# Optimization experiments

Measured on AMD Instinct MI355X. Metric: run time of the kernel, lower is better.

The kernel has to match this reference:

```python
import jax, jax.numpy as jnp
import numpy as np

# 4x4 Walsh-Hadamard matrix in natural (Hadamard/Kronecker) order: H4 = H2 (x) H2
_H4 = jnp.array([[1, 1, 1, 1],
                 [1, -1, 1, -1],
                 [1, 1, -1, -1],
                 [1, -1, -1, 1]], dtype=jnp.float32)

T = 16          # number of 2D WHT coefficients (4x4 block)
BLK = 4         # spatial block size


def _iwht_stream(trans, weight):
    """trans: (16, B, nH, nW, C); weight: (16, C, K) -> out: (B, 4*nH, 4*nW, K).

    Per-coefficient channel mixing in the transform domain, then inverse 2D
    Walsh-Hadamard transform (separable, scale 1/16) back to spatial domain.
    """
    _, B, nH, nW, C = trans.shape
    K = weight.shape[2]
    # transform-domain channel mixing: (t,b,h,w,c) x (t,c,k) -> (t,b,h,w,k)
    mixed = jnp.einsum('tbhwc,tck->tbhwk', trans, weight)
    # split coefficient index t = 4*u + v (row/col frequency)
    mixed = mixed.reshape(BLK, BLK, B, nH, nW, K)
    # inverse separable WHT: out[b,nh,i,nw,j,k] = (1/16) sum_{u,v} H4[i,u] H4[j,v] mixed[u,v,...]
    out = jnp.einsum('iu,jv,uvbhwk->bhiwjk', _H4, _H4, mixed) * (1.0 / 16.0)
    return out.reshape(B, nH * BLK, nW * BLK, K)


def setup_inputs() -> dict:
    key = jax.random.key(0)
    k1, k2, k3, k4 = jax.random.split(key, 4)
    B, nH, nW, C = 16, 28, 28, 64
    out_channels = 128
    K1 = out_channels // 2
    K2 = out_channels // 2 + out_channels % 2
    transIm1 = jax.random.normal(k1, (T, B, nH, nW, C), dtype=jnp.float32)
    transIm2 = jax.random.normal(k2, (T, B, nH, nW, C), dtype=jnp.float32)
    weight1 = jax.random.normal(k3, (T, C, K1), dtype=jnp.float32) * 0.02
    weight2 = jax.random.normal(k4, (T, C, K2), dtype=jnp.float32) * 0.02
    bias1 = jnp.zeros((1, 1, 1, K1), dtype=jnp.float32)
    bias2 = jnp.zeros((1, 1, 1, K2), dtype=jnp.float32)
    return {"transIm1": transIm1, "transIm2": transIm2,
            "weight1": weight1, "weight2": weight2,
            "bias1": bias1, "bias2": bias2}


def reference(transIm1, transIm2, weight1, weight2, bias1, bias2):
    out1 = _iwht_stream(transIm1, weight1) + bias1
    out2 = _iwht_stream(transIm2, weight2) + bias2
    return (out1, out2)
```

## Files before the change

kernel.cpp:

```cpp
#include <hip/hip_runtime.h>
#include <hip/hip_bf16.h>

typedef float f32x4 __attribute__((ext_vector_type(4)));
typedef short s16x8 __attribute__((ext_vector_type(8)));

#define NPIX       12544
#define OUT_STRIDE 12845056
#define NTILES     1568
#define GRIDX      512

__device__ __forceinline__ unsigned short f2bf(float x) {
    union { float f; unsigned u; } un; un.f = x;
    unsigned r = un.u + 0x7FFFu + ((un.u >> 16) & 1u);
    return (unsigned short)(r >> 16);
}

__device__ __forceinline__ short bfs(float x) {
    __hip_bfloat16 h = __float2bfloat16(x);
    return *reinterpret_cast<short*>(&h);
}

__device__ __forceinline__ void gload_lds16(const void* g, void* l) {
    __builtin_amdgcn_global_load_lds(
        (const __attribute__((address_space(1))) unsigned int*)g,
        (__attribute__((address_space(3))) unsigned int*)l, 16, 0, 0);
}

__global__ __launch_bounds__(256) void repack_weights(
        const float* __restrict__ w1, const float* __restrict__ w2,
        unsigned short* __restrict__ wf) {
    int gid = blockIdx.x * 256 + threadIdx.x;
    int k = gid & 63;
    int c = (gid >> 6) & 63;
    int t = (gid >> 12) & 15;
    int s = (gid >> 16) & 1;
    const float* __restrict__ w = s ? w2 : w1;
    float val = w[gid & 65535] * 0.0625f;
    int e = c & 7, lhi = (c >> 3) & 3, ks = c >> 5;
    int l  = lhi * 16 + (k & 15);
    int nt = k >> 4;
    int dst = ((((s * 16 + t) * 2 + ks) * 4 + nt) * 64 + l) * 8 + e;
    wf[dst] = f2bf(val);
}

__global__ __launch_bounds__(256, 2) void iwht_main(
        const float* __restrict__ trans1, const float* __restrict__ trans2,
        const unsigned short* __restrict__ wf,
        const float* __restrict__ bias1, const float* __restrict__ bias2,
        float* __restrict__ out) {
    __shared__ __align__(16) unsigned char lds[65536];

    const int tid  = threadIdx.x;
    const int wid  = tid >> 6;
    const int lane = tid & 63;
    const int lrow = lane & 15;
    const int lhi  = lane >> 4;
    const int bx   = blockIdx.x;

    const int   kk  = wid * 16 + lrow;
    const float bk1 = bias1[kk];
    const float bk2 = bias2[kk];

    const int M = ((NTILES - bx + GRIDX - 1) / GRIDX) * 2;

    const int qsrc = (wid >> 1) * 32 + lhi * 8 + (wid & 1) * 4;
    const s16x8* __restrict__ wbbase = (const s16x8*)wf + (size_t)wid * 64 + lane;

    auto stage_half = [&](int m) {
        const int tau = bx + (m >> 1) * GRIDX;
        const int hf  = m & 1;
        const int s   = (tau >= 784) ? 1 : 0;
        const int bid = tau - s * 784;
        const float* __restrict__ tr = s ? trans2 : trans1;
        const float* g0 = tr + (size_t)(bid * 16 + lrow) * 64 + qsrc;
        unsigned char* db = lds + (m & 1) * 32768 + wid * 1024;
        #pragma unroll
        for (int tt = 0; tt < 8; ++tt) {
            const int t = hf * 8 + tt;
            gload_lds16(g0 + (size_t)t * (NPIX * 64), db + tt * 4096);
        }
    };

    f32x4 o[4][4];
    #pragma unroll
    for (int i = 0; i < 4; ++i)
        #pragma unroll
        for (int j = 0; j < 4; ++j)
            o[i][j] = (f32x4){0.f, 0.f, 0.f, 0.f};

    s16x8 bH[16];

    stage_half(0);

    #pragma unroll 1
    for (int m = 0; m < M; ++m) {
        const int tau = bx + (m >> 1) * GRIDX;
        const int hf  = m & 1;
        const int s   = (tau >= 784) ? 1 : 0;
        const int bid = tau - s * 784;

        {
            const s16x8* __restrict__ wb = wbbase + (size_t)s * 8192;
            #pragma unroll
            for (int tt = 0; tt < 8; ++tt) {
                const int t = hf * 8 + tt;
                bH[tt * 2 + 0] = wb[(size_t)(t * 2 + 0) * 256];
                bH[tt * 2 + 1] = wb[(size_t)(t * 2 + 1) * 256];
            }
        }

        if (m + 1 < M) {
            stage_half(m + 1);
            asm volatile("s_waitcnt vmcnt(8)" ::: "memory");
        } else {
            asm volatile("s_waitcnt vmcnt(0)" ::: "memory");
        }
        __builtin_amdgcn_sched_barrier(0);
        __builtin_amdgcn_s_barrier();

        const unsigned char* __restrict__ hb = lds + (m & 1) * 32768;
        #pragma unroll
        for (int g = 0; g < 2; ++g) {
            f32x4 acc[4];
            #pragma unroll
            for (int v = 0; v < 4; ++v) {
                const int tt = g * 4 + v;
                const unsigned char* ab = hb + tt * 4096 + lane * 16;
                f32x4 q0 = *(const f32x4*)(ab);
                f32x4 q1 = *(const f32x4*)(ab + 1024);
                f32x4 q2 = *(const f32x4*)(ab + 2048);
                f32x4 q3 = *(const f32x4*)(ab + 3072);
                s16x8 a0, a1;
                #pragma unroll
                for (int e = 0; e < 4; ++e) {
                    a0[e] = bfs(q0[e]); a0[4 + e] = bfs(q1[e]);
                    a1[e] = bfs(q2[e]); a1[4 + e] = bfs(q3[e]);
                }
                f32x4 tacc = {0.f, 0.f, 0.f, 0.f};
                tacc = __builtin_amdgcn_mfma_f32_16x16x32_bf16(a0, bH[tt * 2 + 0], tacc, 0, 0, 0);
                tacc = __builtin_amdgcn_mfma_f32_16x16x32_bf16(a1, bH[tt * 2 + 1], tacc, 0, 0, 0);
                acc[v] = tacc;
            }
            f32x4 e0 = acc[0] + acc[1], e1 = acc[0] - acc[1];
            f32x4 e2 = acc[2] + acc[3], e3 = acc[2] - acc[3];
            f32x4 g0 = e0 + e2, g1 = e1 + e3, g2 = e0 - e2, g3 = e1 - e3;
            const int u = hf * 2 + g;
            const float s1 = (u & 1) ? -1.f : 1.f;
            const float s2 = (u & 2) ? -1.f : 1.f;
            const float s3 = s1 * s2;
            #pragma unroll
            for (int j = 0; j < 4; ++j) {
                f32x4 gj = (j == 0) ? g0 : ((j == 1) ? g1 : ((j == 2) ? g2 : g3));
                o[0][j] += gj;
                o[1][j] += s1 * gj;
                o[2][j] += s2 * gj;
                o[3][j] += s3 * gj;
            }
        }

        if (hf) {
            const float bk = s ? bk2 : bk1;
            const int bimg = bid / 49;
            const int hw0  = (bid % 49) * 16;
            float* __restrict__ outp = out + (s ? (size_t)OUT_STRIDE : 0);
            size_t rbase[4];
            #pragma unroll
            for (int r = 0; r < 4; ++r) {
                int hw = hw0 + lhi * 4 + r;
                int h = hw / 28, w = hw % 28;
                rbase[r] = ((size_t)(bimg * 112 + h * 4) * 112 + (w * 4)) * 64 + kk;
            }
            #pragma unroll
            for (int i = 0; i < 4; ++i)
                #pragma unroll
                for (int j = 0; j < 4; ++j) {
                    #pragma unroll
                    for (int r = 0; r < 4; ++r)
                        outp[rbase[r] + (size_t)((i * 112 + j) * 64)] = o[i][j][r] + bk;
                    o[i][j] = (f32x4){0.f, 0.f, 0.f, 0.f};
                }
        }

        __builtin_amdgcn_s_barrier();
    }
}

extern "C" void kernel_launch(void* const* d_in, const int* in_sizes, int n_in,
                              void* d_out, int out_size, void* d_ws, size_t ws_size,
                              hipStream_t stream) {
    const float* t1 = (const float*)d_in[0];
    const float* t2 = (const float*)d_in[1];
    const float* w1 = (const float*)d_in[2];
    const float* w2 = (const float*)d_in[3];
    const float* b1 = (const float*)d_in[4];
    const float* b2 = (const float*)d_in[5];
    unsigned short* wfrag = (unsigned short*)d_ws;
    float* out = (float*)d_out;

    repack_weights<<<dim3(512), dim3(256), 0, stream>>>(w1, w2, wfrag);
    iwht_main<<<dim3(GRIDX), dim3(256), 0, stream>>>(t1, t2, wfrag, b1, b2, out);
}
```

Before: 204.8 us.

## Use one tile per block and stage output through swizzled LDS for vector stores

Replaces the persistent 512-block loop with a 1568-block grid where each block handles a single tile, issuing both halves of its input loads up front. The output is first written into LDS with an XOR swizzle, then read back so each wave writes a full contiguous 1KB row with 16-byte stores, instead of the earlier scattered 4-byte stores. This targets poorly coalesced output writes and lets the hardware scheduler balance work across blocks. In exchange it adds an LDS round trip and extra barriers, and it loses cross-tile overlap of loads with compute inside a block.

After: 197.0 us. 3.8% less time.

```diff
diff --git a/kernel.cpp b/kernel.cpp
--- a/kernel.cpp
+++ b/kernel.cpp
@@ -6,8 +6,6 @@
 
 #define NPIX       12544
 #define OUT_STRIDE 12845056
-#define NTILES     1568
-#define GRIDX      512
 
 __device__ __forceinline__ unsigned short f2bf(float x) {
     union { float f; unsigned u; } un; un.f = x;
@@ -55,31 +53,44 @@
     const int lane = tid & 63;
     const int lrow = lane & 15;
     const int lhi  = lane >> 4;
-    const int bx   = blockIdx.x;
 
-    const int   kk  = wid * 16 + lrow;
-    const float bk1 = bias1[kk];
-    const float bk2 = bias2[kk];
-
-    const int M = ((NTILES - bx + GRIDX - 1) / GRIDX) * 2;
+    const int tau = blockIdx.x;
+    const int s   = (tau >= 784) ? 1 : 0;
+    const int bid = tau - s * 784;
+    const float* __restrict__ trans = s ? trans2 : trans1;
+    const int   kk = wid * 16 + lrow;
+    const float bk = (s ? bias2 : bias1)[kk];
 
     const int qsrc = (wid >> 1) * 32 + lhi * 8 + (wid & 1) * 4;
-    const s16x8* __restrict__ wbbase = (const s16x8*)wf + (size_t)wid * 64 + lane;
+    const float* __restrict__ g0 = trans + (size_t)(bid * 16 + lrow) * 64 + qsrc;
 
-    auto stage_half = [&](int m) {
-        const int tau = bx + (m >> 1) * GRIDX;
-        const int hf  = m & 1;
-        const int s   = (tau >= 784) ? 1 : 0;
-        const int bid = tau - s * 784;
-        const float* __restrict__ tr = s ? trans2 : trans1;
-        const float* g0 = tr + (size_t)(bid * 16 + lrow) * 64 + qsrc;
-        unsigned char* db = lds + (m & 1) * 32768 + wid * 1024;
-        #pragma unroll
-        for (int tt = 0; tt < 8; ++tt) {
-            const int t = hf * 8 + tt;
-            gload_lds16(g0 + (size_t)t * (NPIX * 64), db + tt * 4096);
-        }
-    };
+    #pragma unroll
+    for (int tt = 0; tt < 8; ++tt)
+        gload_lds16(g0 + (size_t)tt * (NPIX * 64), lds + wid * 1024 + tt * 4096);
+
+    const s16x8* __restrict__ wb = (const s16x8*)wf + (size_t)s * 8192 + wid * 64 + lane;
+    s16x8 bE[16];
+    #pragma unroll
+    for (int tt = 0; tt < 8; ++tt) {
+        bE[tt * 2 + 0] = wb[(size_t)(tt * 2 + 0) * 256];
+        bE[tt * 2 + 1] = wb[(size_t)(tt * 2 + 1) * 256];
+    }
+
+    #pragma unroll
+    for (int tt = 0; tt < 8; ++tt)
+        gload_lds16(g0 + (size_t)(8 + tt) * (NPIX * 64),
+                    lds + 32768 + wid * 1024 + tt * 4096);
+
+    asm volatile("s_waitcnt vmcnt(8)" ::: "memory");
+    __builtin_amdgcn_sched_barrier(0);
+    __builtin_amdgcn_s_barrier();
+
+    s16x8 bO[16];
+    #pragma unroll
+    for (int tt = 0; tt < 8; ++tt) {
+        bO[tt * 2 + 0] = wb[(size_t)((8 + tt) * 2 + 0) * 256];
+        bO[tt * 2 + 1] = wb[(size_t)((8 + tt) * 2 + 1) * 256];
+    }
 
     f32x4 o[4][4];
     #pragma unroll
@@ -88,37 +99,7 @@
         for (int j = 0; j < 4; ++j)
             o[i][j] = (f32x4){0.f, 0.f, 0.f, 0.f};
 
-    s16x8 bH[16];
-
-    stage_half(0);
-
-    #pragma unroll 1
-    for (int m = 0; m < M; ++m) {
-        const int tau = bx + (m >> 1) * GRIDX;
-        const int hf  = m & 1;
-        const int s   = (tau >= 784) ? 1 : 0;
-        const int bid = tau - s * 784;
-
-        {
-            const s16x8* __restrict__ wb = wbbase + (size_t)s * 8192;
-            #pragma unroll
-            for (int tt = 0; tt < 8; ++tt) {
-                const int t = hf * 8 + tt;
-                bH[tt * 2 + 0] = wb[(size_t)(t * 2 + 0) * 256];
-                bH[tt * 2 + 1] = wb[(size_t)(t * 2 + 1) * 256];
-            }
-        }
-
-        if (m + 1 < M) {
-            stage_half(m + 1);
-            asm volatile("s_waitcnt vmcnt(8)" ::: "memory");
-        } else {
-            asm volatile("s_waitcnt vmcnt(0)" ::: "memory");
-        }
-        __builtin_amdgcn_sched_barrier(0);
-        __builtin_amdgcn_s_barrier();
-
-        const unsigned char* __restrict__ hb = lds + (m & 1) * 32768;
+    auto compute_half = [&](const unsigned char* hb, const s16x8 (&bb)[16], int ubase) {
         #pragma unroll
         for (int g = 0; g < 2; ++g) {
             f32x4 acc[4];
@@ -137,51 +118,63 @@
                     a1[e] = bfs(q2[e]); a1[4 + e] = bfs(q3[e]);
                 }
                 f32x4 tacc = {0.f, 0.f, 0.f, 0.f};
-                tacc = __builtin_amdgcn_mfma_f32_16x16x32_bf16(a0, bH[tt * 2 + 0], tacc, 0, 0, 0);
-                tacc = __builtin_amdgcn_mfma_f32_16x16x32_bf16(a1, bH[tt * 2 + 1], tacc, 0, 0, 0);
+                tacc = __builtin_amdgcn_mfma_f32_16x16x32_bf16(a0, bb[tt * 2 + 0], tacc, 0, 0, 0);
+                tacc = __builtin_amdgcn_mfma_f32_16x16x32_bf16(a1, bb[tt * 2 + 1], tacc, 0, 0, 0);
                 acc[v] = tacc;
             }
             f32x4 e0 = acc[0] + acc[1], e1 = acc[0] - acc[1];
             f32x4 e2 = acc[2] + acc[3], e3 = acc[2] - acc[3];
-            f32x4 g0 = e0 + e2, g1 = e1 + e3, g2 = e0 - e2, g3 = e1 - e3;
-            const int u = hf * 2 + g;
+            f32x4 g0v = e0 + e2, g1v = e1 + e3, g2v = e0 - e2, g3v = e1 - e3;
+            const int u = ubase + g;
             const float s1 = (u & 1) ? -1.f : 1.f;
             const float s2 = (u & 2) ? -1.f : 1.f;
             const float s3 = s1 * s2;
             #pragma unroll
             for (int j = 0; j < 4; ++j) {
-                f32x4 gj = (j == 0) ? g0 : ((j == 1) ? g1 : ((j == 2) ? g2 : g3));
+                f32x4 gj = (j == 0) ? g0v : ((j == 1) ? g1v : ((j == 2) ? g2v : g3v));
                 o[0][j] += gj;
                 o[1][j] += s1 * gj;
                 o[2][j] += s2 * gj;
                 o[3][j] += s3 * gj;
             }
         }
+    };
 
-        if (hf) {
-            const float bk = s ? bk2 : bk1;
-            const int bimg = bid / 49;
-            const int hw0  = (bid % 49) * 16;
-            float* __restrict__ outp = out + (s ? (size_t)OUT_STRIDE : 0);
-            size_t rbase[4];
+    compute_half(lds, bE, 0);
+
+    asm volatile("s_waitcnt vmcnt(0)" ::: "memory");
+    __builtin_amdgcn_sched_barrier(0);
+    __builtin_amdgcn_s_barrier();
+
+    compute_half(lds + 32768, bO, 2);
+
+    __builtin_amdgcn_s_barrier();
+    #pragma unroll
+    for (int i = 0; i < 4; ++i)
+        #pragma unroll
+        for (int r = 0; r < 4; ++r) {
+            const int p = lhi * 4 + r;
+            unsigned char* base = lds + i * 16384 + p * 1024;
+            const int swz = (p & 7) << 4;
             #pragma unroll
-            for (int r = 0; r < 4; ++r) {
-                int hw = hw0 + lhi * 4 + r;
-                int h = hw / 28, w = hw % 28;
-                rbase[r] = ((size_t)(bimg * 112 + h * 4) * 112 + (w * 4)) * 64 + kk;
-            }
-            #pragma unroll
-            for (int i = 0; i < 4; ++i)
-                #pragma unroll
-                for (int j = 0; j < 4; ++j) {
-                    #pragma unroll
-                    for (int r = 0; r < 4; ++r)
-                        outp[rbase[r] + (size_t)((i * 112 + j) * 64)] = o[i][j][r] + bk;
-                    o[i][j] = (f32x4){0.f, 0.f, 0.f, 0.f};
-                }
+            for (int j = 0; j < 4; ++j)
+                *(float*)(base + ((j * 256 + kk * 4) ^ swz)) = o[i][j][r] + bk;
         }
+    asm volatile("s_waitcnt lgkmcnt(0)" ::: "memory");
+    __builtin_amdgcn_sched_barrier(0);
+    __builtin_amdgcn_s_barrier();
 
-        __builtin_amdgcn_s_barrier();
+    const int bimg = bid / 49;
+    const int hw0  = (bid % 49) * 16;
+    float* __restrict__ outp = out + (s ? (size_t)OUT_STRIDE : 0);
+    #pragma unroll
+    for (int n = 0; n < 16; ++n) {
+        f32x4 v = *(const f32x4*)(lds + wid * 16384 + n * 1024
+                                  + ((lane * 16) ^ ((n & 7) << 4)));
+        const int hw = hw0 + n;
+        const int h = hw / 28, w = hw % 28;
+        *(f32x4*)(outp + ((size_t)(bimg * 112 + h * 4 + wid) * 112 + w * 4) * 64
+                  + lane * 4) = v;
     }
 }
 
@@ -198,5 +191,5 @@
     float* out = (float*)d_out;
 
     repack_weights<<<dim3(512), dim3(256), 0, stream>>>(w1, w2, wfrag);
-    iwht_main<<<dim3(GRIDX), dim3(256), 0, stream>>>(t1, t2, wfrag, b1, b2, out);
+    iwht_main<<<dim3(1568), dim3(256), 0, stream>>>(t1, t2, wfrag, b1, b2, out);
 }
```
